# Kernel tuning notes

Hardware: AMD Instinct MI355X
Metric: run time of the kernel (lower is better)

The kernel has to match this reference:

```python
import jax, jax.numpy as jnp
import numpy as np

# BasicLS (deep_gnss): batched weighted least squares x_hat = pinv(W A) (W r)
# with W = diag(ones) == identity, so WA == A and Wr == r mathematically.
# A = [-los_x, -los_y, -los_z, 1] per measurement, r = pseudorange residual.

B = 262144  # batch of GNSS epochs
M = 32      # satellite measurements per epoch
DIM = 4     # [residual, los_x, los_y, los_z]


def setup_inputs() -> dict:
    key = jax.random.key(0)
    kx, _ = jax.random.split(key)
    x = jax.random.normal(kx, (B, M, DIM), dtype=jnp.float32)
    pad_mask = jnp.zeros((B, M), dtype=bool)  # unused by the module's forward
    return {"x": x, "pad_mask": pad_mask}


def reference(x, pad_mask):
    Bb, Mm, _ = x.shape
    # A: [B, M, 4] = concat(-x[:,:,1:4], ones)
    A = jnp.concatenate([-x[:, :, 1:4], jnp.ones((Bb, Mm, 1), dtype=x.dtype)], axis=-1)
    r = x[:, :, 0:1]  # [B, M, 1]
    # W = diag_embed(ones) is the identity, so WA = A and Wr = r.
    A_pinv = jnp.linalg.pinv(A)          # [B, 4, M] (SVD-based, matches torch.pinverse)
    out = jnp.matmul(A_pinv, r)[..., 0]  # [B, 4]
    return out
```

## Files before the change

kernel.cpp:

```cpp
#include <hip/hip_runtime.h>


#define GLOBAL_AS __attribute__((address_space(1)))
#define LDS_AS    __attribute__((address_space(3)))

__device__ __forceinline__ void async_copy16(const float4* gptr, float4* lptr) {
    __builtin_amdgcn_global_load_lds((const GLOBAL_AS void*)gptr,
                                     (LDS_AS void*)lptr, 16, 0, 0);
}

__global__ __launch_bounds__(256) void basicls_kernel(const float* __restrict__ x,
                                                      float* __restrict__ out) {
    __shared__ float4 tile[4 * 512];

    const int tid = threadIdx.x;
    const int w   = tid >> 6;
    const int t   = tid & 63;
    const int b0  = blockIdx.x * 64;

    const float4* src = reinterpret_cast<const float4*>(x) + (size_t)(b0 + w * 16) * 32;
    float4* chunk = tile + w * 512;
#pragma unroll
    for (int k = 0; k < 8; ++k) {
        async_copy16(src + k * 64 + t, chunk + k * 64);
    }
    __syncthreads();

    const int g   = t >> 2;
    const int sub = t & 3;

    float s11 = 0.f, s12 = 0.f, s13 = 0.f, s22 = 0.f, s23 = 0.f, s33 = 0.f;
    float s1 = 0.f, s2 = 0.f, s3 = 0.f;
    float t1 = 0.f, t2 = 0.f, t3 = 0.f, t0 = 0.f;

#pragma unroll
    for (int j = 0; j < 8; ++j) {
        int jj = (j + g) & 7;
        float4 v = chunk[g * 32 + sub * 8 + jj];
        float r  = v.x;
        float a1 = v.y, a2 = v.z, a3 = v.w;
        s11 = fmaf(a1, a1, s11);
        s12 = fmaf(a1, a2, s12);
        s13 = fmaf(a1, a3, s13);
        s22 = fmaf(a2, a2, s22);
        s23 = fmaf(a2, a3, s23);
        s33 = fmaf(a3, a3, s33);
        s1 += a1; s2 += a2; s3 += a3;
        t1 = fmaf(a1, r, t1);
        t2 = fmaf(a2, r, t2);
        t3 = fmaf(a3, r, t3);
        t0 += r;
    }

#define QUAD_REDUCE(v) \
    v += __shfl_xor(v, 1); \
    v += __shfl_xor(v, 2);
    QUAD_REDUCE(s11) QUAD_REDUCE(s12) QUAD_REDUCE(s13)
    QUAD_REDUCE(s22) QUAD_REDUCE(s23) QUAD_REDUCE(s33)
    QUAD_REDUCE(s1)  QUAD_REDUCE(s2)  QUAD_REDUCE(s3)
    QUAD_REDUCE(t1)  QUAD_REDUCE(t2)  QUAD_REDUCE(t3)
    QUAD_REDUCE(t0)
#undef QUAD_REDUCE

    float G[4][4];
    G[0][0] = s11; G[0][1] = s12; G[0][2] = s13; G[0][3] = -s1;
    G[1][0] = s12; G[1][1] = s22; G[1][2] = s23; G[1][3] = -s2;
    G[2][0] = s13; G[2][1] = s23; G[2][2] = s33; G[2][3] = -s3;
    G[3][0] = -s1; G[3][1] = -s2; G[3][2] = -s3; G[3][3] = 32.0f;
    float rhs[4] = { -t1, -t2, -t3, t0 };

    float L[4][4];
#pragma unroll
    for (int k = 0; k < 4; ++k) {
        float d = G[k][k];
#pragma unroll
        for (int j = 0; j < 4; ++j) {
            if (j < k) d = fmaf(-L[k][j], L[k][j], d);
        }
        float lkk = sqrtf(fmaxf(d, 1e-30f));
        L[k][k] = lkk;
        float inv = __frcp_rn(lkk);
#pragma unroll
        for (int i = 0; i < 4; ++i) {
            if (i > k) {
                float s = G[i][k];
#pragma unroll
                for (int j = 0; j < 4; ++j) {
                    if (j < k) s = fmaf(-L[i][j], L[k][j], s);
                }
                L[i][k] = s * inv;
            }
        }
    }

    float y[4];
#pragma unroll
    for (int i = 0; i < 4; ++i) {
        float s = rhs[i];
#pragma unroll
        for (int j = 0; j < 4; ++j) {
            if (j < i) s = fmaf(-L[i][j], y[j], s);
        }
        y[i] = s * __frcp_rn(L[i][i]);
    }

    float wv[4];
#pragma unroll
    for (int i = 3; i >= 0; --i) {
        float s = y[i];
#pragma unroll
        for (int j = 0; j < 4; ++j) {
            if (j > i) s = fmaf(-L[j][i], wv[j], s);
        }
        wv[i] = s * __frcp_rn(L[i][i]);
    }

    if (sub == 0) {
        int b = b0 + w * 16 + g;
        reinterpret_cast<float4*>(out)[b] = make_float4(wv[0], wv[1], wv[2], wv[3]);
    }
}

extern "C" void kernel_launch(void* const* d_in, const int* in_sizes, int n_in,
                              void* d_out, int out_size, void* d_ws, size_t ws_size,
                              hipStream_t stream) {
    const float* x = (const float*)d_in[0];
    float* out = (float*)d_out;
    int B = in_sizes[0] / (32 * 4);
    dim3 block(256);
    dim3 grid(B / 64);
    basicls_kernel<<<grid, block, 0, stream>>>(x, out);
}
```

Before: 199.2 us.

## Double-buffer per-wave LDS tiles to overlap async loads with solves

Each wave now processes four 16-epoch tiles in sequence, using two LDS buffers. The next tile's async global-to-LDS copy is issued before the current tile is solved, with explicit vmcnt waits in place of a block-wide barrier. The grid shrinks fourfold to match. The goal is to hide load latency behind the Gram-matrix and Cholesky compute. The cost is double the LDS per block, which lowers occupancy and the number of loads in flight across the machine. The scheme also relies on hand-placed waitcnt counts being correct.

```diff
diff --git a/kernel.cpp b/kernel.cpp
--- a/kernel.cpp
+++ b/kernel.cpp
@@ -9,26 +9,15 @@
                                      (LDS_AS void*)lptr, 16, 0, 0);
 }
 
-__global__ __launch_bounds__(256) void basicls_kernel(const float* __restrict__ x,
-                                                      float* __restrict__ out) {
-    __shared__ float4 tile[4 * 512];
-
-    const int tid = threadIdx.x;
-    const int w   = tid >> 6;
-    const int t   = tid & 63;
-    const int b0  = blockIdx.x * 64;
-
-    const float4* src = reinterpret_cast<const float4*>(x) + (size_t)(b0 + w * 16) * 32;
-    float4* chunk = tile + w * 512;
+__device__ __forceinline__ void stage_tile(const float4* src, float4* dst, int t) {
 #pragma unroll
     for (int k = 0; k < 8; ++k) {
-        async_copy16(src + k * 64 + t, chunk + k * 64);
+        async_copy16(src + k * 64 + t, dst + k * 64);
     }
-    __syncthreads();
+}
 
-    const int g   = t >> 2;
-    const int sub = t & 3;
-
+__device__ __forceinline__ void solve_tile(const float4* chunk, int g, int sub,
+                                           int b, float* __restrict__ out) {
     float s11 = 0.f, s12 = 0.f, s13 = 0.f, s22 = 0.f, s23 = 0.f, s33 = 0.f;
     float s1 = 0.f, s2 = 0.f, s3 = 0.f;
     float t1 = 0.f, t2 = 0.f, t3 = 0.f, t0 = 0.f;
@@ -116,9 +105,52 @@
     }
 
     if (sub == 0) {
-        int b = b0 + w * 16 + g;
         reinterpret_cast<float4*>(out)[b] = make_float4(wv[0], wv[1], wv[2], wv[3]);
     }
+}
+
+#define WAIT_VMCNT_8() do {                                   \
+        asm volatile("s_waitcnt vmcnt(8)" ::: "memory");      \
+        __builtin_amdgcn_sched_barrier(0);                    \
+    } while (0)
+#define WAIT_VMCNT_0() do {                                   \
+        asm volatile("s_waitcnt vmcnt(0)" ::: "memory");      \
+        __builtin_amdgcn_sched_barrier(0);                    \
+    } while (0)
+
+__global__ __launch_bounds__(256) void basicls_kernel(const float* __restrict__ x,
+                                                      float* __restrict__ out) {
+    __shared__ float4 tile[4 * 2 * 512];
+
+    const int tid = threadIdx.x;
+    const int w   = tid >> 6;
+    const int t   = tid & 63;
+    const int g   = t >> 2;
+    const int sub = t & 3;
+
+    const int wgid = blockIdx.x * 4 + w;
+    const float4* src = reinterpret_cast<const float4*>(x) + (size_t)wgid * 2048;
+    const int bbase = wgid * 64;
+
+    float4* buf0 = tile + w * 1024;
+    float4* buf1 = buf0 + 512;
+
+    stage_tile(src, buf0, t);
+
+    stage_tile(src + 512, buf1, t);
+    WAIT_VMCNT_8();
+    solve_tile(buf0, g, sub, bbase + g, out);
+
+    stage_tile(src + 1024, buf0, t);
+    WAIT_VMCNT_8();
+    solve_tile(buf1, g, sub, bbase + 16 + g, out);
+
+    stage_tile(src + 1536, buf1, t);
+    WAIT_VMCNT_8();
+    solve_tile(buf0, g, sub, bbase + 32 + g, out);
+
+    WAIT_VMCNT_0();
+    solve_tile(buf1, g, sub, bbase + 48 + g, out);
 }
 
 extern "C" void kernel_launch(void* const* d_in, const int* in_sizes, int n_in,
@@ -128,6 +160,6 @@
     float* out = (float*)d_out;
     int B = in_sizes[0] / (32 * 4);
     dim3 block(256);
-    dim3 grid(B / 64);
+    dim3 grid(B / 256);
     basicls_kernel<<<grid, block, 0, stream>>>(x, out);
 }
```

Measured after the change: 201.0 us. No clear change (+0.9%).
